# Kernel tuning notes

Hardware: AMD Instinct MI355X
Metric: run time of the kernel (lower is better)

## Reference

```python
import jax, jax.numpy as jnp
import numpy as np

B, D_IN, D_H = 32768, 512, 512


def setup_inputs() -> dict:
    key = jax.random.key(0)
    ks = jax.random.split(key, 7)
    s_in = 1.0 / np.sqrt(D_IN)
    s_h = 1.0 / np.sqrt(D_H)
    x = jax.random.normal(ks[0], (B, D_IN), dtype=jnp.float32)
    C = jax.random.normal(ks[1], (B, D_H), dtype=jnp.float32)
    h = jax.random.normal(ks[2], (B, D_H), dtype=jnp.float32)
    # Concatenated gate weights: order [i, f, o, g]. Each gate has its own
    # independent Linear(input_dim->hidden) and Linear(hidden->hidden) in torch;
    # stacking them column-wise gives identical math with 2 GEMMs.
    Wx = jax.random.uniform(ks[3], (D_IN, 4 * D_H), dtype=jnp.float32, minval=-s_in, maxval=s_in)
    bx = jax.random.uniform(ks[4], (4 * D_H,), dtype=jnp.float32, minval=-s_in, maxval=s_in)
    Wh = jax.random.uniform(ks[5], (D_H, 4 * D_H), dtype=jnp.float32, minval=-s_h, maxval=s_h)
    bh = jax.random.uniform(ks[6], (4 * D_H,), dtype=jnp.float32, minval=-s_h, maxval=s_h)
    return {"x": x, "C": C, "h": h, "Wx": Wx, "bx": bx, "Wh": Wh, "bh": bh}


def reference(x, C, h, Wx, bx, Wh, bh):
    # Two fused GEMMs replace the 8 small Linear calls (same math).
    z = x @ Wx + bx + h @ Wh + bh  # [B, 4H]
    i, f, o, g = jnp.split(z, 4, axis=-1)
    i = jax.nn.sigmoid(i)
    f = jax.nn.sigmoid(f)
    o = jax.nn.sigmoid(o)
    g = jnp.tanh(g)
    C_new = f * C + i * g
    h_new = o * jnp.tanh(C_new)
    return (C_new, h_new)
```

## Files before the change

### kernel.cpp

```cpp
#include <hip/hip_runtime.h>
#include <stdint.h>


#define BROWS 32768
#define DH 512
#define KTOT 1024
#define BM 128
#define BK 64

typedef __attribute__((ext_vector_type(8))) __bf16 bf16x8;
typedef __attribute__((ext_vector_type(4))) float f32x4;
typedef __attribute__((address_space(1))) void gvoid;
typedef __attribute__((address_space(3))) void lvoid;

__device__ __forceinline__ void gl_lds16(const void* g, void* l) {
  __builtin_amdgcn_global_load_lds((gvoid*)g, (lvoid*)l, 16, 0, 0);
}

__device__ __forceinline__ float sigf(float v)  { return 1.0f / (1.0f + __expf(-v)); }
__device__ __forceinline__ float tanhf_(float v){ return 1.0f - 2.0f / (1.0f + __expf(2.0f * v)); }

__global__ void conv_xh(const float* __restrict__ x, const float* __restrict__ h,
                        __bf16* __restrict__ xh) {
  int o = blockIdx.x * 256 + threadIdx.x;
  int c = (o & 127) * 8;
  int r = o >> 7;
  const float* src = (c < DH) ? (x + (size_t)r * DH + c)
                              : (h + (size_t)r * DH + (c - DH));
  float4 f0 = *(const float4*)src;
  float4 f1 = *(const float4*)(src + 4);
  bf16x8 v;
  v[0] = (__bf16)f0.x; v[1] = (__bf16)f0.y; v[2] = (__bf16)f0.z; v[3] = (__bf16)f0.w;
  v[4] = (__bf16)f1.x; v[5] = (__bf16)f1.y; v[6] = (__bf16)f1.z; v[7] = (__bf16)f1.w;
  *(bf16x8*)(xh + (size_t)o * 8) = v;
}

__global__ void pack_w(const float* __restrict__ Wx, const float* __restrict__ Wh,
                       __bf16* __restrict__ Wt) {
  __shared__ __bf16 T[128][72];
  const int jb = blockIdx.y;
  const int k0 = blockIdx.x * 64;
  const float* Wsrc = (k0 < DH) ? (Wx + (size_t)k0 * 4 * DH)
                                : (Wh + (size_t)(k0 - DH) * 4 * DH);
  const int t = threadIdx.x;
  const int s = t & 31, kr0 = t >> 5;
  const int g = s >> 3, q = s & 7;
  const int r0 = (q >> 2) * 64 + g * 16 + (q & 3) * 4;
  #pragma unroll
  for (int it = 0; it < 8; ++it) {
    int kr = it * 8 + kr0;
    float4 f = *(const float4*)(Wsrc + (size_t)kr * 4 * DH + g * DH + jb * 32 + q * 4);
    T[r0 + 0][kr] = (__bf16)f.x;
    T[r0 + 1][kr] = (__bf16)f.y;
    T[r0 + 2][kr] = (__bf16)f.z;
    T[r0 + 3][kr] = (__bf16)f.w;
  }
  __syncthreads();
  #pragma unroll
  for (int it = 0; it < 4; ++it) {
    int lin = it * 256 + t;
    int r = lin >> 3, k8 = lin & 7;
    bf16x8 v;
    #pragma unroll
    for (int j = 0; j < 8; ++j) v[j] = T[r][k8 * 8 + j];
    *(bf16x8*)(Wt + (size_t)(jb * 128 + r) * KTOT + k0 + k8 * 8) = v;
  }
}

__global__ __launch_bounds__(256, 3) void lstm_gemm2(
    const __bf16* __restrict__ xh, const __bf16* __restrict__ Wt,
    const float* __restrict__ bx, const float* __restrict__ bh,
    const float* __restrict__ Cin, float* __restrict__ out) {
  __shared__ __attribute__((aligned(16))) __bf16 As[BM * BK];
  __shared__ __attribute__((aligned(16))) __bf16 Bs[BM * BK];

  const int tid  = threadIdx.x;
  const int lane = tid & 63;
  const int wave = tid >> 6;
  const int wm = wave >> 1, wn = wave & 1;
  const int jb   = blockIdx.x;
  const int row0 = blockIdx.y * BM;

  const __bf16* Bt = Wt + (size_t)jb * 128 * KTOT;

  const int hd = jb * 32 + wn * 16 + (lane & 15);
  float bias[4], cpv[4][4];
  #pragma unroll
  for (int g = 0; g < 4; ++g) bias[g] = bx[g * DH + hd] + bh[g * DH + hd];
  #pragma unroll
  for (int cm = 0; cm < 4; ++cm)
    #pragma unroll
    for (int i2 = 0; i2 < 4; ++i2)
      cpv[cm][i2] = Cin[(size_t)(row0 + wm * 64 + cm * 16 + (lane >> 4) * 4 + i2) * DH + hd];

  f32x4 acc[4][4];
  #pragma unroll
  for (int a_ = 0; a_ < 4; ++a_)
    #pragma unroll
    for (int b_ = 0; b_ < 4; ++b_) acc[a_][b_] = (f32x4)0.0f;

  for (int k0 = 0; k0 < KTOT; k0 += BK) {
    #pragma unroll
    for (int it = 0; it < 4; ++it) {
      int lin = it * 256 + tid;
      int r = lin >> 3, c8 = lin & 7;
      int cs = c8 ^ (r & 7);
      gl_lds16(xh + (size_t)(row0 + r) * KTOT + k0 + cs * 8, &As[lin * 8]);
    }
    #pragma unroll
    for (int it = 0; it < 4; ++it) {
      int lin = it * 256 + tid;
      int r = lin >> 3, c8 = lin & 7;
      int cs = c8 ^ (r & 7);
      gl_lds16(Bt + (size_t)r * KTOT + k0 + cs * 8, &Bs[lin * 8]);
    }
    __syncthreads();

    #pragma unroll
    for (int ks = 0; ks < 2; ++ks) {
      const int q = lane >> 4;
      bf16x8 af[4], bfr[4];
      #pragma unroll
      for (int cm = 0; cm < 4; ++cm) {
        int row = wm * 64 + cm * 16 + (lane & 15);
        int cc = (ks * 4 + q) ^ (row & 7);
        af[cm] = *(const bf16x8*)&As[row * BK + cc * 8];
      }
      #pragma unroll
      for (int cn = 0; cn < 4; ++cn) {
        int row = wn * 64 + cn * 16 + (lane & 15);
        int cc = (ks * 4 + q) ^ (row & 7);
        bfr[cn] = *(const bf16x8*)&Bs[row * BK + cc * 8];
      }
      #pragma unroll
      for (int cm = 0; cm < 4; ++cm)
        #pragma unroll
        for (int cn = 0; cn < 4; ++cn)
          acc[cm][cn] = __builtin_amdgcn_mfma_f32_16x16x32_bf16(
              af[cm], bfr[cn], acc[cm][cn], 0, 0, 0);
    }
    __syncthreads();
  }

  #pragma unroll
  for (int cm = 0; cm < 4; ++cm) {
    const int rbase = row0 + wm * 64 + cm * 16 + (lane >> 4) * 4;
    #pragma unroll
    for (int i2 = 0; i2 < 4; ++i2) {
      const size_t r = (size_t)(rbase + i2);
      float ig = sigf(acc[cm][0][i2] + bias[0]);
      float fg = sigf(acc[cm][1][i2] + bias[1]);
      float og = sigf(acc[cm][2][i2] + bias[2]);
      float gg = tanhf_(acc[cm][3][i2] + bias[3]);
      float cnew = fg * cpv[cm][i2] + ig * gg;
      float hnew = og * tanhf_(cnew);
      out[r * DH + hd] = cnew;
      out[(size_t)BROWS * DH + r * DH + hd] = hnew;
    }
  }
}

__global__ __launch_bounds__(256, 3) void lstm_gemm(
    const float* __restrict__ x, const float* __restrict__ h,
    const __bf16* __restrict__ Wt, const float* __restrict__ bx,
    const float* __restrict__ bh, const float* __restrict__ Cin,
    float* __restrict__ out) {
  __shared__ __attribute__((aligned(16))) __bf16 As[BM * BK];
  __shared__ __attribute__((aligned(16))) __bf16 Bs[BM * BK];
  const int tid  = threadIdx.x;
  const int lane = tid & 63;
  const int wave = tid >> 6;
  const int wm = wave >> 1, wn = wave & 1;
  const int jb   = blockIdx.x;
  const int row0 = blockIdx.y * BM;
  const __bf16* Bt = Wt + (size_t)jb * 128 * KTOT;
  f32x4 acc[4][4];
  #pragma unroll
  for (int a_ = 0; a_ < 4; ++a_)
    #pragma unroll
    for (int b_ = 0; b_ < 4; ++b_) acc[a_][b_] = (f32x4)0.0f;
  for (int k0 = 0; k0 < KTOT; k0 += BK) {
    const float* Aptr = (k0 < DH) ? (x + (size_t)row0 * DH + k0)
                                  : (h + (size_t)row0 * DH + (k0 - DH));
    bf16x8 ta[4], tb[4];
    #pragma unroll
    for (int it = 0; it < 4; ++it) {
      int lin = it * 256 + tid;
      int r = lin >> 3, c8 = lin & 7;
      const float* src = Aptr + r * DH + c8 * 8;
      float4 f0 = *(const float4*)src;
      float4 f1 = *(const float4*)(src + 4);
      bf16x8 v;
      v[0] = (__bf16)f0.x; v[1] = (__bf16)f0.y; v[2] = (__bf16)f0.z; v[3] = (__bf16)f0.w;
      v[4] = (__bf16)f1.x; v[5] = (__bf16)f1.y; v[6] = (__bf16)f1.z; v[7] = (__bf16)f1.w;
      ta[it] = v;
      tb[it] = *(const bf16x8*)(Bt + (size_t)r * KTOT + k0 + c8 * 8);
    }
    #pragma unroll
    for (int it = 0; it < 4; ++it) {
      int lin = it * 256 + tid;
      *(bf16x8*)&As[lin * 8] = ta[it];
      *(bf16x8*)&Bs[lin * 8] = tb[it];
    }
    __syncthreads();
    #pragma unroll
    for (int ks = 0; ks < 2; ++ks) {
      const int ko = ks * 32 + (lane >> 4) * 8;
      bf16x8 af[4], bfr[4];
      #pragma unroll
      for (int cm = 0; cm < 4; ++cm)
        af[cm] = *(const bf16x8*)&As[(wm * 64 + cm * 16 + (lane & 15)) * BK + ko];
      #pragma unroll
      for (int cn = 0; cn < 4; ++cn)
        bfr[cn] = *(const bf16x8*)&Bs[(wn * 64 + cn * 16 + (lane & 15)) * BK + ko];
      #pragma unroll
      for (int cm = 0; cm < 4; ++cm)
        #pragma unroll
        for (int cn = 0; cn < 4; ++cn)
          acc[cm][cn] = __builtin_amdgcn_mfma_f32_16x16x32_bf16(
              af[cm], bfr[cn], acc[cm][cn], 0, 0, 0);
    }
    __syncthreads();
  }
  const int hd = jb * 32 + wn * 16 + (lane & 15);
  float bias[4];
  #pragma unroll
  for (int g2 = 0; g2 < 4; ++g2) bias[g2] = bx[g2 * DH + hd] + bh[g2 * DH + hd];
  #pragma unroll
  for (int cm = 0; cm < 4; ++cm) {
    const int rbase = row0 + wm * 64 + cm * 16 + (lane >> 4) * 4;
    #pragma unroll
    for (int i2 = 0; i2 < 4; ++i2) {
      const size_t r = (size_t)(rbase + i2);
      float ig = sigf(acc[cm][0][i2] + bias[0]);
      float fg = sigf(acc[cm][1][i2] + bias[1]);
      float og = sigf(acc[cm][2][i2] + bias[2]);
      float gg = tanhf_(acc[cm][3][i2] + bias[3]);
      float cp = Cin[r * DH + hd];
      float cnew = fg * cp + ig * gg;
      float hnew = og * tanhf_(cnew);
      out[r * DH + hd] = cnew;
      out[(size_t)BROWS * DH + r * DH + hd] = hnew;
    }
  }
}

__global__ void lstm_naive(const float* __restrict__ x, const float* __restrict__ Cin,
                           const float* __restrict__ h, const float* __restrict__ Wx,
                           const float* __restrict__ bxp, const float* __restrict__ Wh,
                           const float* __restrict__ bhp, float* __restrict__ out) {
  int idx = blockIdx.x * 256 + threadIdx.x;
  int r = idx >> 9, hd = idx & 511;
  float z[4];
  #pragma unroll
  for (int g = 0; g < 4; ++g) z[g] = bxp[g * DH + hd] + bhp[g * DH + hd];
  for (int k = 0; k < DH; ++k) {
    float xv = x[(size_t)r * DH + k];
    #pragma unroll
    for (int g = 0; g < 4; ++g) z[g] += xv * Wx[k * 4 * DH + g * DH + hd];
  }
  for (int k = 0; k < DH; ++k) {
    float hv = h[(size_t)r * DH + k];
    #pragma unroll
    for (int g = 0; g < 4; ++g) z[g] += hv * Wh[k * 4 * DH + g * DH + hd];
  }
  float ig = sigf(z[0]), fg = sigf(z[1]), og = sigf(z[2]), gg = tanhf_(z[3]);
  float cp = Cin[(size_t)r * DH + hd];
  float cnew = fg * cp + ig * gg;
  float hnew = og * tanhf_(cnew);
  out[(size_t)r * DH + hd] = cnew;
  out[(size_t)BROWS * DH + (size_t)r * DH + hd] = hnew;
}

extern "C" void kernel_launch(void* const* d_in, const int* in_sizes, int n_in,
                              void* d_out, int out_size, void* d_ws, size_t ws_size,
                              hipStream_t stream) {
  const float* x  = (const float*)d_in[0];
  const float* Ci = (const float*)d_in[1];
  const float* h  = (const float*)d_in[2];
  const float* Wx = (const float*)d_in[3];
  const float* bx = (const float*)d_in[4];
  const float* Wh = (const float*)d_in[5];
  const float* bh = (const float*)d_in[6];
  float* out = (float*)d_out;

  const size_t wt_bytes = (size_t)2048 * KTOT * sizeof(__bf16);
  const size_t xh_bytes = (size_t)BROWS * KTOT * sizeof(__bf16);

  if (ws_size >= wt_bytes + xh_bytes) {
    __bf16* Wt = (__bf16*)d_ws;
    __bf16* xh = (__bf16*)((char*)d_ws + wt_bytes);
    pack_w<<<dim3(16, 16), dim3(256), 0, stream>>>(Wx, Wh, Wt);
    conv_xh<<<dim3((BROWS * KTOT / 8) / 256), dim3(256), 0, stream>>>(x, h, xh);
    lstm_gemm2<<<dim3(16, BROWS / BM), dim3(256), 0, stream>>>(xh, Wt, bx, bh, Ci, out);
  } else if (ws_size >= wt_bytes) {
    __bf16* Wt = (__bf16*)d_ws;
    pack_w<<<dim3(16, 16), dim3(256), 0, stream>>>(Wx, Wh, Wt);
    lstm_gemm<<<dim3(16, BROWS / BM), dim3(256), 0, stream>>>(x, h, Wt, bx, bh, Ci, out);
  } else {
    lstm_naive<<<dim3((BROWS * DH) / 256), dim3(256), 0, stream>>>(
        x, Ci, h, Wx, bx, Wh, bh, out);
  }
}
```

Before: 422.8 us.

## Replace GEMM with 256x256 double-buffered LDS pipeline and interleaved MFMA phases

Replaces the 128x128 single-buffered bf16 GEMM with a 256x256 tile kernel using 8 waves, double-buffered LDS, and direct global-to-LDS loads for the next K tile. These loads are staged in quarters between MFMA phases, with explicit barriers, waitcnts and setprio. The aim is to overlap memory traffic with MFMA work, remove the serial load-then-compute stall, and raise reuse per loaded byte. The epilogue loads C late and writes outputs with nontemporal stores. It costs much more register and LDS pressure (128 KB of LDS) and adds hand-managed waitcnt counts that must be exactly right.

```diff
diff --git a/kernel.cpp b/kernel.cpp
--- a/kernel.cpp
+++ b/kernel.cpp
@@ -67,95 +67,131 @@
   }
 }
 
-__global__ __launch_bounds__(256, 3) void lstm_gemm2(
+#define SB __builtin_amdgcn_sched_barrier(0)
+#define PH_PRE do { SB; __builtin_amdgcn_s_barrier(); \
+  asm volatile("s_waitcnt lgkmcnt(0)" ::: "memory"); SB; } while (0)
+#define PH_POST do { SB; __builtin_amdgcn_s_barrier(); SB; } while (0)
+#define PH_POST_VM do { SB; asm volatile("s_waitcnt vmcnt(0)" ::: "memory"); \
+  __builtin_amdgcn_s_barrier(); SB; } while (0)
+
+#define STAGE_A4(PN_, kk_) do { \
+  _Pragma("unroll") \
+  for (int s_ = 0; s_ < 4; ++s_) { \
+    const int r_ = s_ * 64 + sr; \
+    gl_lds16(xh + (size_t)(row0 + r_) * KTOT + (kk_) + cs8 * 8, \
+             &As[PN_][(s_ * 512 + tid) * 8]); \
+  } } while (0)
+
+#define STAGE_B2(PN_, kk_, h_) do { \
+  _Pragma("unroll") \
+  for (int s_ = 2 * (h_); s_ < 2 * (h_) + 2; ++s_) { \
+    const int r_ = s_ * 64 + sr; \
+    gl_lds16(Bt + (size_t)r_ * KTOT + (kk_) + cs8 * 8, \
+             &Bs[PN_][(s_ * 512 + tid) * 8]); \
+  } } while (0)
+
+#define DS_A4(P_, cmb_, ks_) do { \
+  const int cc_ = ((ks_) * 4 + q) ^ (l15 & 7); \
+  _Pragma("unroll") \
+  for (int i_ = 0; i_ < 4; ++i_) { \
+    const int row_ = wm * 128 + ((cmb_) + i_) * 16 + l15; \
+    af[i_] = *(const bf16x8*)&As[P_][row_ * 64 + cc_ * 8]; \
+  } } while (0)
+
+#define DS_B4(P_, ks_) do { \
+  const int cc_ = ((ks_) * 4 + q) ^ (l15 & 7); \
+  _Pragma("unroll") \
+  for (int i_ = 0; i_ < 4; ++i_) { \
+    const int row_ = wn * 64 + i_ * 16 + l15; \
+    bfr[i_] = *(const bf16x8*)&Bs[P_][row_ * 64 + cc_ * 8]; \
+  } } while (0)
+
+#define MFMA16(cmb_) do { \
+  __builtin_amdgcn_s_setprio(1); \
+  _Pragma("unroll") \
+  for (int i_ = 0; i_ < 4; ++i_) \
+    _Pragma("unroll") \
+    for (int j_ = 0; j_ < 4; ++j_) \
+      acc[(cmb_) + i_][j_] = __builtin_amdgcn_mfma_f32_16x16x32_bf16( \
+          af[i_], bfr[j_], acc[(cmb_) + i_][j_], 0, 0, 0); \
+  __builtin_amdgcn_s_setprio(0); \
+} while (0)
+
+#define TILE(T_, P_, PN_, DOST_) do { \
+  bf16x8 af[4], bfr[4]; \
+   \
+  DS_B4(P_, 0); DS_A4(P_, 0, 0); \
+  if (DOST_) STAGE_A4(PN_, ((T_) + 1) * BK); \
+  PH_PRE; MFMA16(0); PH_POST; \
+   \
+  DS_A4(P_, 4, 0); \
+  if (DOST_) STAGE_B2(PN_, ((T_) + 1) * BK, 0); \
+  PH_PRE; MFMA16(4); PH_POST; \
+   \
+  DS_B4(P_, 1); DS_A4(P_, 0, 1); \
+  if (DOST_) STAGE_B2(PN_, ((T_) + 1) * BK, 1); \
+  PH_PRE; MFMA16(0); PH_POST; \
+   \
+  DS_A4(P_, 4, 1); \
+  PH_PRE; MFMA16(4); PH_POST_VM; \
+} while (0)
+
+__global__ __launch_bounds__(512, 2) void lstm_gemm3(
     const __bf16* __restrict__ xh, const __bf16* __restrict__ Wt,
     const float* __restrict__ bx, const float* __restrict__ bh,
     const float* __restrict__ Cin, float* __restrict__ out) {
-  __shared__ __attribute__((aligned(16))) __bf16 As[BM * BK];
-  __shared__ __attribute__((aligned(16))) __bf16 Bs[BM * BK];
+  __shared__ __attribute__((aligned(16))) __bf16 As[2][256 * 64];
+  __shared__ __attribute__((aligned(16))) __bf16 Bs[2][256 * 64];
 
   const int tid  = threadIdx.x;
   const int lane = tid & 63;
   const int wave = tid >> 6;
-  const int wm = wave >> 1, wn = wave & 1;
+  const int wm = wave >> 2, wn = wave & 3;
+  const int q = lane >> 4, l15 = lane & 15;
   const int jb   = blockIdx.x;
-  const int row0 = blockIdx.y * BM;
-
-  const __bf16* Bt = Wt + (size_t)jb * 128 * KTOT;
-
-  const int hd = jb * 32 + wn * 16 + (lane & 15);
-  float bias[4], cpv[4][4];
+  const int row0 = blockIdx.y * 256;
+
+  const __bf16* Bt = Wt + (size_t)jb * 256 * KTOT;
+
+  const int sr  = tid >> 3;
+  const int cs8 = (tid & 7) ^ (sr & 7);
+
+  const int hd = jb * 64 + wn * 16 + l15;
+  float bias[4];
   #pragma unroll
   for (int g = 0; g < 4; ++g) bias[g] = bx[g * DH + hd] + bh[g * DH + hd];
-  #pragma unroll
-  for (int cm = 0; cm < 4; ++cm)
-    #pragma unroll
-    for (int i2 = 0; i2 < 4; ++i2)
-      cpv[cm][i2] = Cin[(size_t)(row0 + wm * 64 + cm * 16 + (lane >> 4) * 4 + i2) * DH + hd];
-
-  f32x4 acc[4][4];
-  #pragma unroll
-  for (int a_ = 0; a_ < 4; ++a_)
+
+  f32x4 acc[8][4];
+  #pragma unroll
+  for (int a_ = 0; a_ < 8; ++a_)
     #pragma unroll
     for (int b_ = 0; b_ < 4; ++b_) acc[a_][b_] = (f32x4)0.0f;
 
-  for (int k0 = 0; k0 < KTOT; k0 += BK) {
-    #pragma unroll
-    for (int it = 0; it < 4; ++it) {
-      int lin = it * 256 + tid;
-      int r = lin >> 3, c8 = lin & 7;
-      int cs = c8 ^ (r & 7);
-      gl_lds16(xh + (size_t)(row0 + r) * KTOT + k0 + cs * 8, &As[lin * 8]);
-    }
-    #pragma unroll
-    for (int it = 0; it < 4; ++it) {
-      int lin = it * 256 + tid;
-      int r = lin >> 3, c8 = lin & 7;
-      int cs = c8 ^ (r & 7);
-      gl_lds16(Bt + (size_t)r * KTOT + k0 + cs * 8, &Bs[lin * 8]);
-    }
-    __syncthreads();
-
-    #pragma unroll
-    for (int ks = 0; ks < 2; ++ks) {
-      const int q = lane >> 4;
-      bf16x8 af[4], bfr[4];
-      #pragma unroll
-      for (int cm = 0; cm < 4; ++cm) {
-        int row = wm * 64 + cm * 16 + (lane & 15);
-        int cc = (ks * 4 + q) ^ (row & 7);
-        af[cm] = *(const bf16x8*)&As[row * BK + cc * 8];
-      }
-      #pragma unroll
-      for (int cn = 0; cn < 4; ++cn) {
-        int row = wn * 64 + cn * 16 + (lane & 15);
-        int cc = (ks * 4 + q) ^ (row & 7);
-        bfr[cn] = *(const bf16x8*)&Bs[row * BK + cc * 8];
-      }
-      #pragma unroll
-      for (int cm = 0; cm < 4; ++cm)
-        #pragma unroll
-        for (int cn = 0; cn < 4; ++cn)
-          acc[cm][cn] = __builtin_amdgcn_mfma_f32_16x16x32_bf16(
-              af[cm], bfr[cn], acc[cm][cn], 0, 0, 0);
-    }
-    __syncthreads();
-  }
-
-  #pragma unroll
-  for (int cm = 0; cm < 4; ++cm) {
-    const int rbase = row0 + wm * 64 + cm * 16 + (lane >> 4) * 4;
+  STAGE_A4(0, 0); STAGE_B2(0, 0, 0); STAGE_B2(0, 0, 1);
+  STAGE_A4(1, BK); STAGE_B2(1, BK, 0); STAGE_B2(1, BK, 1);
+  asm volatile("s_waitcnt vmcnt(8)" ::: "memory");
+  __builtin_amdgcn_s_barrier();
+
+  for (int tt = 0; tt < 16; tt += 2) {
+    TILE(tt,     0, 1, (tt > 0));
+    TILE(tt + 1, 1, 0, (tt < 14));
+  }
+
+  #pragma unroll
+  for (int cm = 0; cm < 8; ++cm) {
+    const int rbase = row0 + wm * 128 + cm * 16 + q * 4;
     #pragma unroll
     for (int i2 = 0; i2 < 4; ++i2) {
       const size_t r = (size_t)(rbase + i2);
+      float cp = Cin[r * DH + hd];
       float ig = sigf(acc[cm][0][i2] + bias[0]);
       float fg = sigf(acc[cm][1][i2] + bias[1]);
       float og = sigf(acc[cm][2][i2] + bias[2]);
       float gg = tanhf_(acc[cm][3][i2] + bias[3]);
-      float cnew = fg * cpv[cm][i2] + ig * gg;
+      float cnew = fg * cp + ig * gg;
       float hnew = og * tanhf_(cnew);
-      out[r * DH + hd] = cnew;
-      out[(size_t)BROWS * DH + r * DH + hd] = hnew;
+      __builtin_nontemporal_store(cnew, &out[r * DH + hd]);
+      __builtin_nontemporal_store(hnew, &out[(size_t)BROWS * DH + r * DH + hd]);
     }
   }
 }
@@ -165,8 +201,8 @@
     const __bf16* __restrict__ Wt, const float* __restrict__ bx,
     const float* __restrict__ bh, const float* __restrict__ Cin,
     float* __restrict__ out) {
-  __shared__ __attribute__((aligned(16))) __bf16 As[BM * BK];
-  __shared__ __attribute__((aligned(16))) __bf16 Bs[BM * BK];
+  __shared__ __attribute__((aligned(16))) __bf16 Asf[BM * BK];
+  __shared__ __attribute__((aligned(16))) __bf16 Bsf[BM * BK];
   const int tid  = threadIdx.x;
   const int lane = tid & 63;
   const int wave = tid >> 6;
@@ -199,8 +235,8 @@
     #pragma unroll
     for (int it = 0; it < 4; ++it) {
       int lin = it * 256 + tid;
-      *(bf16x8*)&As[lin * 8] = ta[it];
-      *(bf16x8*)&Bs[lin * 8] = tb[it];
+      *(bf16x8*)&Asf[lin * 8] = ta[it];
+      *(bf16x8*)&Bsf[lin * 8] = tb[it];
     }
     __syncthreads();
     #pragma unroll
@@ -209,10 +245,10 @@
       bf16x8 af[4], bfr[4];
       #pragma unroll
       for (int cm = 0; cm < 4; ++cm)
-        af[cm] = *(const bf16x8*)&As[(wm * 64 + cm * 16 + (lane & 15)) * BK + ko];
+        af[cm] = *(const bf16x8*)&Asf[(wm * 64 + cm * 16 + (lane & 15)) * BK + ko];
       #pragma unroll
       for (int cn = 0; cn < 4; ++cn)
-        bfr[cn] = *(const bf16x8*)&Bs[(wn * 64 + cn * 16 + (lane & 15)) * BK + ko];
+        bfr[cn] = *(const bf16x8*)&Bsf[(wn * 64 + cn * 16 + (lane & 15)) * BK + ko];
       #pragma unroll
       for (int cm = 0; cm < 4; ++cm)
         #pragma unroll
@@ -292,7 +328,7 @@
     __bf16* xh = (__bf16*)((char*)d_ws + wt_bytes);
     pack_w<<<dim3(16, 16), dim3(256), 0, stream>>>(Wx, Wh, Wt);
     conv_xh<<<dim3((BROWS * KTOT / 8) / 256), dim3(256), 0, stream>>>(x, h, xh);
-    lstm_gemm2<<<dim3(16, BROWS / BM), dim3(256), 0, stream>>>(xh, Wt, bx, bh, Ci, out);
+    lstm_gemm3<<<dim3(8, BROWS / 256), dim3(512), 0, stream>>>(xh, Wt, bx, bh, Ci, out);
   } else if (ws_size >= wt_bytes) {
     __bf16* Wt = (__bf16*)d_ws;
     pack_w<<<dim3(16, 16), dim3(256), 0, stream>>>(Wx, Wh, Wt);
```

New measurement: 468.8 us. 10.9% more time.

## Fuse fp32-to-bf16 activation conversion into GEMM with register prefetch and XCD remap

Applied to the files above, without the earlier changes.

Removes the separate conv_xh pass that wrote a bf16 copy of x and h to workspace. The GEMM kernel now loads fp32 x/h tiles directly, prefetching the next K-tile into registers during the MFMA work, and converts them to bf16 when storing to LDS. It also remaps workgroup IDs so blocks sharing row tiles are grouped per XCD, and uses nontemporal stores for the outputs. The aim is to cut the extra full read/write of activations and one kernel launch, at the cost of higher register pressure and doubled fp32 global read bytes inside the GEMM.

```diff
diff --git a/kernel.cpp b/kernel.cpp
--- a/kernel.cpp
+++ b/kernel.cpp
@@ -19,21 +19,6 @@
 
 __device__ __forceinline__ float sigf(float v)  { return 1.0f / (1.0f + __expf(-v)); }
 __device__ __forceinline__ float tanhf_(float v){ return 1.0f - 2.0f / (1.0f + __expf(2.0f * v)); }
-
-__global__ void conv_xh(const float* __restrict__ x, const float* __restrict__ h,
-                        __bf16* __restrict__ xh) {
-  int o = blockIdx.x * 256 + threadIdx.x;
-  int c = (o & 127) * 8;
-  int r = o >> 7;
-  const float* src = (c < DH) ? (x + (size_t)r * DH + c)
-                              : (h + (size_t)r * DH + (c - DH));
-  float4 f0 = *(const float4*)src;
-  float4 f1 = *(const float4*)(src + 4);
-  bf16x8 v;
-  v[0] = (__bf16)f0.x; v[1] = (__bf16)f0.y; v[2] = (__bf16)f0.z; v[3] = (__bf16)f0.w;
-  v[4] = (__bf16)f1.x; v[5] = (__bf16)f1.y; v[6] = (__bf16)f1.z; v[7] = (__bf16)f1.w;
-  *(bf16x8*)(xh + (size_t)o * 8) = v;
-}
 
 __global__ void pack_w(const float* __restrict__ Wx, const float* __restrict__ Wh,
                        __bf16* __restrict__ Wt) {
@@ -67,10 +52,11 @@
   }
 }
 
-__global__ __launch_bounds__(256, 3) void lstm_gemm2(
-    const __bf16* __restrict__ xh, const __bf16* __restrict__ Wt,
-    const float* __restrict__ bx, const float* __restrict__ bh,
-    const float* __restrict__ Cin, float* __restrict__ out) {
+__global__ __launch_bounds__(256, 3) void lstm_fused(
+    const float* __restrict__ x, const float* __restrict__ h,
+    const __bf16* __restrict__ Wt, const float* __restrict__ bx,
+    const float* __restrict__ bh, const float* __restrict__ Cin,
+    float* __restrict__ out) {
   __shared__ __attribute__((aligned(16))) __bf16 As[BM * BK];
   __shared__ __attribute__((aligned(16))) __bf16 Bs[BM * BK];
 
@@ -78,10 +64,34 @@
   const int lane = tid & 63;
   const int wave = tid >> 6;
   const int wm = wave >> 1, wn = wave & 1;
-  const int jb   = blockIdx.x;
-  const int row0 = blockIdx.y * BM;
+
+  const int wgid = blockIdx.y * 16 + blockIdx.x;
+  const int lin  = (wgid & 7) * 512 + (wgid >> 3);
+  const int jb   = lin & 15;
+  const int row0 = (lin >> 4) * BM;
 
   const __bf16* Bt = Wt + (size_t)jb * 128 * KTOT;
+  const float*  Ax = x + (size_t)row0 * DH;
+  const float*  Ah = h + (size_t)row0 * DH;
+
+  int sr_[4], sc_[4];
+  #pragma unroll
+  for (int it = 0; it < 4; ++it) {
+    int l2 = it * 256 + tid;
+    sr_[it] = l2 >> 3;
+    sc_[it] = (l2 & 7) ^ (sr_[it] & 7);
+  }
+
+  float4 pf[4][2];
+  {
+    const float* base = Ax;
+    #pragma unroll
+    for (int it = 0; it < 4; ++it) {
+      const float* s = base + (size_t)sr_[it] * DH + sc_[it] * 8;
+      pf[it][0] = *(const float4*)s;
+      pf[it][1] = *(const float4*)(s + 4);
+    }
+  }
 
   const int hd = jb * 32 + wn * 16 + (lane & 15);
   float bias[4], cpv[4][4];
@@ -102,19 +112,29 @@
   for (int k0 = 0; k0 < KTOT; k0 += BK) {
     #pragma unroll
     for (int it = 0; it < 4; ++it) {
-      int lin = it * 256 + tid;
-      int r = lin >> 3, c8 = lin & 7;
-      int cs = c8 ^ (r & 7);
-      gl_lds16(xh + (size_t)(row0 + r) * KTOT + k0 + cs * 8, &As[lin * 8]);
-    }
-    #pragma unroll
-    for (int it = 0; it < 4; ++it) {
-      int lin = it * 256 + tid;
-      int r = lin >> 3, c8 = lin & 7;
-      int cs = c8 ^ (r & 7);
-      gl_lds16(Bt + (size_t)r * KTOT + k0 + cs * 8, &Bs[lin * 8]);
-    }
+      bf16x8 v;
+      v[0] = (__bf16)pf[it][0].x; v[1] = (__bf16)pf[it][0].y;
+      v[2] = (__bf16)pf[it][0].z; v[3] = (__bf16)pf[it][0].w;
+      v[4] = (__bf16)pf[it][1].x; v[5] = (__bf16)pf[it][1].y;
+      v[6] = (__bf16)pf[it][1].z; v[7] = (__bf16)pf[it][1].w;
+      *(bf16x8*)&As[(it * 256 + tid) * 8] = v;
+    }
+    #pragma unroll
+    for (int it = 0; it < 4; ++it)
+      gl_lds16(Bt + (size_t)sr_[it] * KTOT + k0 + sc_[it] * 8,
+               &Bs[(it * 256 + tid) * 8]);
     __syncthreads();
+
+    if (k0 + BK < KTOT) {
+      const int kn = k0 + BK;
+      const float* base = (kn < DH) ? (Ax + kn) : (Ah + (kn - DH));
+      #pragma unroll
+      for (int it = 0; it < 4; ++it) {
+        const float* s = base + (size_t)sr_[it] * DH + sc_[it] * 8;
+        pf[it][0] = *(const float4*)s;
+        pf[it][1] = *(const float4*)(s + 4);
+      }
+    }
 
     #pragma unroll
     for (int ks = 0; ks < 2; ++ks) {
@@ -154,93 +174,8 @@
       float gg = tanhf_(acc[cm][3][i2] + bias[3]);
       float cnew = fg * cpv[cm][i2] + ig * gg;
       float hnew = og * tanhf_(cnew);
-      out[r * DH + hd] = cnew;
-      out[(size_t)BROWS * DH + r * DH + hd] = hnew;
-    }
-  }
-}
-
-__global__ __launch_bounds__(256, 3) void lstm_gemm(
-    const float* __restrict__ x, const float* __restrict__ h,
-    const __bf16* __restrict__ Wt, const float* __restrict__ bx,
-    const float* __restrict__ bh, const float* __restrict__ Cin,
-    float* __restrict__ out) {
-  __shared__ __attribute__((aligned(16))) __bf16 As[BM * BK];
-  __shared__ __attribute__((aligned(16))) __bf16 Bs[BM * BK];
-  const int tid  = threadIdx.x;
-  const int lane = tid & 63;
-  const int wave = tid >> 6;
-  const int wm = wave >> 1, wn = wave & 1;
-  const int jb   = blockIdx.x;
-  const int row0 = blockIdx.y * BM;
-  const __bf16* Bt = Wt + (size_t)jb * 128 * KTOT;
-  f32x4 acc[4][4];
-  #pragma unroll
-  for (int a_ = 0; a_ < 4; ++a_)
-    #pragma unroll
-    for (int b_ = 0; b_ < 4; ++b_) acc[a_][b_] = (f32x4)0.0f;
-  for (int k0 = 0; k0 < KTOT; k0 += BK) {
-    const float* Aptr = (k0 < DH) ? (x + (size_t)row0 * DH + k0)
-                                  : (h + (size_t)row0 * DH + (k0 - DH));
-    bf16x8 ta[4], tb[4];
-    #pragma unroll
-    for (int it = 0; it < 4; ++it) {
-      int lin = it * 256 + tid;
-      int r = lin >> 3, c8 = lin & 7;
-      const float* src = Aptr + r * DH + c8 * 8;
-      float4 f0 = *(const float4*)src;
-      float4 f1 = *(const float4*)(src + 4);
-      bf16x8 v;
-      v[0] = (__bf16)f0.x; v[1] = (__bf16)f0.y; v[2] = (__bf16)f0.z; v[3] = (__bf16)f0.w;
-      v[4] = (__bf16)f1.x; v[5] = (__bf16)f1.y; v[6] = (__bf16)f1.z; v[7] = (__bf16)f1.w;
-      ta[it] = v;
-      tb[it] = *(const bf16x8*)(Bt + (size_t)r * KTOT + k0 + c8 * 8);
-    }
-    #pragma unroll
-    for (int it = 0; it < 4; ++it) {
-      int lin = it * 256 + tid;
-      *(bf16x8*)&As[lin * 8] = ta[it];
-      *(bf16x8*)&Bs[lin * 8] = tb[it];
-    }
-    __syncthreads();
-    #pragma unroll
-    for (int ks = 0; ks < 2; ++ks) {
-      const int ko = ks * 32 + (lane >> 4) * 8;
-      bf16x8 af[4], bfr[4];
-      #pragma unroll
-      for (int cm = 0; cm < 4; ++cm)
-        af[cm] = *(const bf16x8*)&As[(wm * 64 + cm * 16 + (lane & 15)) * BK + ko];
-      #pragma unroll
-      for (int cn = 0; cn < 4; ++cn)
-        bfr[cn] = *(const bf16x8*)&Bs[(wn * 64 + cn * 16 + (lane & 15)) * BK + ko];
-      #pragma unroll
-      for (int cm = 0; cm < 4; ++cm)
-        #pragma unroll
-        for (int cn = 0; cn < 4; ++cn)
-          acc[cm][cn] = __builtin_amdgcn_mfma_f32_16x16x32_bf16(
-              af[cm], bfr[cn], acc[cm][cn], 0, 0, 0);
-    }
-    __syncthreads();
-  }
-  const int hd = jb * 32 + wn * 16 + (lane & 15);
-  float bias[4];
-  #pragma unroll
-  for (int g2 = 0; g2 < 4; ++g2) bias[g2] = bx[g2 * DH + hd] + bh[g2 * DH + hd];
-  #pragma unroll
-  for (int cm = 0; cm < 4; ++cm) {
-    const int rbase = row0 + wm * 64 + cm * 16 + (lane >> 4) * 4;
-    #pragma unroll
-    for (int i2 = 0; i2 < 4; ++i2) {
-      const size_t r = (size_t)(rbase + i2);
-      float ig = sigf(acc[cm][0][i2] + bias[0]);
-      float fg = sigf(acc[cm][1][i2] + bias[1]);
-      float og = sigf(acc[cm][2][i2] + bias[2]);
-      float gg = tanhf_(acc[cm][3][i2] + bias[3]);
-      float cp = Cin[r * DH + hd];
-      float cnew = fg * cp + ig * gg;
-      float hnew = og * tanhf_(cnew);
-      out[r * DH + hd] = cnew;
-      out[(size_t)BROWS * DH + r * DH + hd] = hnew;
+      __builtin_nontemporal_store(cnew, &out[r * DH + hd]);
+      __builtin_nontemporal_store(hnew, &out[(size_t)BROWS * DH + r * DH + hd]);
     }
   }
 }
@@ -285,18 +220,12 @@
   float* out = (float*)d_out;
 
   const size_t wt_bytes = (size_t)2048 * KTOT * sizeof(__bf16);
-  const size_t xh_bytes = (size_t)BROWS * KTOT * sizeof(__bf16);
-
-  if (ws_size >= wt_bytes + xh_bytes) {
-    __bf16* Wt = (__bf16*)d_ws;
-    __bf16* xh = (__bf16*)((char*)d_ws + wt_bytes);
-    pack_w<<<dim3(16, 16), dim3(256), 0, stream>>>(Wx, Wh, Wt);
-    conv_xh<<<dim3((BROWS * KTOT / 8) / 256), dim3(256), 0, stream>>>(x, h, xh);
-    lstm_gemm2<<<dim3(16, BROWS / BM), dim3(256), 0, stream>>>(xh, Wt, bx, bh, Ci, out);
-  } else if (ws_size >= wt_bytes) {
+
+  if (ws_size >= wt_bytes) {
     __bf16* Wt = (__bf16*)d_ws;
     pack_w<<<dim3(16, 16), dim3(256), 0, stream>>>(Wx, Wh, Wt);
-    lstm_gemm<<<dim3(16, BROWS / BM), dim3(256), 0, stream>>>(x, h, Wt, bx, bh, Ci, out);
+    lstm_fused<<<dim3(16, BROWS / BM), dim3(256), 0, stream>>>(
+        x, h, Wt, bx, bh, Ci, out);
   } else {
     lstm_naive<<<dim3((BROWS * DH) / 256), dim3(256), 0, stream>>>(
         x, Ci, h, Wx, bx, Wh, bh, out);
```

Result: slower. 538.0 us (+27.3%).
